# Optimization experiments

Hardware: AMD Instinct MI355X
Metric: run time of the kernel (lower is better)

## Reference

```python
import jax, jax.numpy as jnp
import numpy as np

GROUP_SIZE = 16
E2M1_MAX = 6.0
# Positive E2M1 grid and midpoints for round-to-nearest
E2M1_POS = jnp.array([0.0, 0.5, 1.0, 1.5, 2.0, 3.0, 4.0, 6.0], jnp.float32)
E2M1_MID = jnp.array([0.25, 0.75, 1.25, 1.75, 2.5, 3.5, 5.0], jnp.float32)
# Full 16-entry signed LUT (bit3 = sign, sign-magnitude)
E2M1_LUT = jnp.array([0.0, 0.5, 1.0, 1.5, 2.0, 3.0, 4.0, 6.0,
                      -0.0, -0.5, -1.0, -1.5, -2.0, -3.0, -4.0, -6.0], jnp.float32)

def _round_e2m1(x):
    # nearest value on the E2M1 grid (clamped to +-6)
    idx = jnp.searchsorted(E2M1_MID, jnp.abs(x))
    return jnp.sign(x) * E2M1_POS[idx]

def nvfp4_act_qdq(x, input_scale):
    # per-group dynamic quantize to NVFP4 with fp8-e4m3 group scale, then dequantize
    orig_shape = x.shape
    xg = x.astype(jnp.float32).reshape(*orig_shape[:-1], -1, GROUP_SIZE)
    amax = jnp.max(jnp.abs(xg), axis=-1, keepdims=True)
    s = (amax / (E2M1_MAX * input_scale)).astype(jnp.float8_e4m3fn).astype(jnp.float32)
    s = jnp.where(s > 0, s, 1.0)
    total = s * input_scale  # effective per-group scale
    dq = _round_e2m1(xg / total) * total
    return dq.reshape(orig_shape).astype(jnp.float16)

def nvfp4_dequantize(weight, weight_scale, weight_scale_2):
    # weight: [O, I//2] packed bytes (values 0..255); low nibble = even index
    O = weight.shape[0]
    low = weight & 0xF
    high = (weight >> 4) & 0xF
    codes = jnp.stack([low, high], axis=-1).reshape(O, -1)  # [O, I]
    vals = E2M1_LUT[codes].reshape(O, -1, GROUP_SIZE)       # [O, G, 16]
    w = vals * weight_scale[:, :, None] * weight_scale_2
    return w.reshape(O, -1).astype(jnp.float16)

def setup_inputs() -> dict:
    key = jax.random.key(0)
    k1, k2, k3 = jax.random.split(key, 3)
    B, S, I, O = 8, 16, 8192, 8192
    hidden_states = jax.random.normal(k1, (B, S, I), dtype=jnp.float16)
    weight = jax.random.randint(k2, (O, I // 2), 0, 256, dtype=jnp.int32)
    weight_scale = jax.random.uniform(k3, (O, I // GROUP_SIZE), dtype=jnp.float32) * 0.05 + 0.001
    weight_scale_2 = jnp.ones((1,), jnp.float32)
    input_scale = jnp.ones((1,), jnp.float32)
    return {"hidden_states": hidden_states, "weight": weight,
            "weight_scale": weight_scale, "weight_scale_2": weight_scale_2,
            "input_scale": input_scale}

def reference(hidden_states, weight, weight_scale, weight_scale_2, input_scale):
    hs_dq = nvfp4_act_qdq(hidden_states, input_scale)
    w_dq = nvfp4_dequantize(weight, weight_scale, weight_scale_2)
    return jnp.matmul(hs_dq, w_dq.T)  # [B, S, O], fp16
```

## Files before the change

kernel.cpp:

```cpp
#include <hip/hip_runtime.h>
#include <stdint.h>


typedef _Float16 half8 __attribute__((ext_vector_type(8)));
typedef float float4v __attribute__((ext_vector_type(4)));

__device__ __forceinline__ uint32_t perm_b32(uint32_t hi, uint32_t lo, uint32_t sel) {
  return __builtin_amdgcn_perm(hi, lo, sel);
}

__device__ __forceinline__ float e4m3_roundtrip(float x) {
  if (x < 0.015625f) {
    return __builtin_rintf(x * 512.0f) * 0.001953125f;
  }
  uint32_t u = __float_as_uint(x);
  u += 0x7FFFFu + ((u >> 20) & 1u);
  u &= 0xFFF00000u;
  float y = __uint_as_float(u);
  return fminf(y, 448.0f);
}

__global__ __launch_bounds__(256)
void aqdq_kernel(const float* __restrict__ hs,
                 const float* __restrict__ isc,
                 uint4* __restrict__ asw) {
  const int t = blockIdx.x * 256 + threadIdx.x;
  const int m = t >> 9;
  const int g = t & 511;
  const float* p = hs + m * 8192 + g * 16;
  float x[16];
#pragma unroll
  for (int q = 0; q < 4; ++q) *(float4*)&x[q * 4] = ((const float4*)p)[q];
  float amax = 0.0f;
#pragma unroll
  for (int i = 0; i < 16; ++i) amax = fmaxf(amax, fabsf(x[i]));

  float is = isc[0];
  float s = e4m3_roundtrip(amax / (6.0f * is));
  if (!(s > 0.0f)) s = 1.0f;
  float total = s * is;

  union { _Float16 h[16]; uint4 v4[2]; } qq;
#pragma unroll
  for (int i = 0; i < 16; ++i) {
    float r = x[i] / total;
    float a = fabsf(r);
    float v = (a <= 0.25f) ? 0.0f
            : (a <= 0.75f) ? 0.5f
            : (a <= 1.25f) ? 1.0f
            : (a <= 1.75f) ? 1.5f
            : (a <= 2.5f)  ? 2.0f
            : (a <= 3.5f)  ? 3.0f
            : (a <= 5.0f)  ? 4.0f : 6.0f;
    qq.h[i] = (_Float16)(copysignf(v, r) * total);
  }
  const int mb = m >> 4;
#pragma unroll
  for (int hf = 0; hf < 2; ++hf) {
    int k = g * 16 + hf * 8;
    int kb = k >> 5;
    int quad = (k >> 3) & 3;
    int lane = (m & 15) | (quad << 4);
    asw[(kb * 8 + mb) * 64 + lane] = qq.v4[hf];
  }
}

__device__ __forceinline__ half8 decode_scale(int4 w, float sf) {
  uint32_t t0 = perm_b32((uint32_t)w.y, (uint32_t)w.x, 0x00000400u);
  uint32_t t1 = perm_b32((uint32_t)w.w, (uint32_t)w.z, 0x04000000u);
  uint32_t b  = perm_b32(t1, t0, 0x07060100u);
  uint32_t ev = b & 0x0F0F0F0Fu;
  uint32_t od = (b >> 4) & 0x0F0F0F0Fu;
  uint32_t evm = ev & 0x07070707u;
  uint32_t odm = od & 0x07070707u;
  uint32_t evs = (ev & 0x08080808u) << 4;
  uint32_t ods = (od & 0x08080808u) << 4;
  uint32_t evh = perm_b32(0x46444240u, 0x3E3C3800u, evm) | evs;
  uint32_t odh = perm_b32(0x46444240u, 0x3E3C3800u, odm) | ods;
  union { uint32_t u[4]; half8 h; } r;
  r.u[0] = perm_b32(odh, evh, 0x04000000u) & 0xFF00FF00u;
  r.u[1] = perm_b32(odh, evh, 0x05000100u) & 0xFF00FF00u;
  r.u[2] = perm_b32(odh, evh, 0x06000200u) & 0xFF00FF00u;
  r.u[3] = perm_b32(odh, evh, 0x07000300u) & 0xFF00FF00u;
  _Float16 hsf = (_Float16)sf;
  half8 sv = {hsf, hsf, hsf, hsf, hsf, hsf, hsf, hsf};
  return r.h * sv;
}

__global__ __launch_bounds__(512)
void gemm_kernel(const uint4* __restrict__ asw,
                 const int* __restrict__ wq,
                 const float* __restrict__ wsc,
                 const float* __restrict__ ws2p,
                 float* __restrict__ out) {
  __shared__ float red[8][32][136];
  const int lane = threadIdx.x & 63;
  const int wv = threadIdx.x >> 6;
  const int quad = lane >> 4;
  const int n0 = blockIdx.x * 32;
  const int rA = n0 + (lane & 15);
  const int rB = rA + 16;
  const float ws2 = ws2p[0];
  const int4* wpA = (const int4*)(wq + rA * 4096);
  const int4* wpB = (const int4*)(wq + rB * 4096);
  const float* wsA = wsc + rA * 512;
  const float* wsB = wsc + rB * 512;
  const int kbase = wv * 1024;

  float4v acc[2][8];
#pragma unroll
  for (int ng = 0; ng < 2; ++ng)
#pragma unroll
    for (int mb = 0; mb < 8; ++mb) acc[ng][mb] = (float4v){0.f, 0.f, 0.f, 0.f};

  const uint4* ap = asw + (kbase >> 5) * 512 + lane;

#pragma unroll 2
  for (int ks = 0; ks < 32; ++ks) {
    const int k0 = kbase + ks * 32;
    const int wi = (k0 >> 3) + quad;
    int4 wA = wpA[wi];
    int4 wB = wpB[wi];
    const int si = (k0 >> 4) + (quad >> 1);
    float sA = wsA[si] * ws2;
    float sB = wsB[si] * ws2;
    uint4 af[8];
#pragma unroll
    for (int mb = 0; mb < 8; ++mb) af[mb] = ap[ks * 512 + mb * 64];
    half8 bA = decode_scale(wA, sA);
    half8 bB = decode_scale(wB, sB);
#pragma unroll
    for (int mb = 0; mb < 8; ++mb) {
      union { uint4 u; half8 h; } a;
      a.u = af[mb];
      acc[0][mb] = __builtin_amdgcn_mfma_f32_16x16x32_f16(a.h, bA, acc[0][mb], 0, 0, 0);
      acc[1][mb] = __builtin_amdgcn_mfma_f32_16x16x32_f16(a.h, bB, acc[1][mb], 0, 0, 0);
    }
  }

#pragma unroll
  for (int ng = 0; ng < 2; ++ng)
#pragma unroll
    for (int mb = 0; mb < 8; ++mb) {
      *(float4v*)&red[wv][ng * 16 + (lane & 15)][mb * 16 + quad * 4] = acc[ng][mb];
    }
  __syncthreads();

  const int t = threadIdx.x;
  const int m = t >> 2;
  const int ng8 = (t & 3) * 8;
  float o[8];
#pragma unroll
  for (int j = 0; j < 8; ++j) {
    float s = 0.f;
#pragma unroll
    for (int p = 0; p < 8; ++p) s += red[p][ng8 + j][m];
    o[j] = s;
  }
  float* op = out + m * 8192 + n0 + ng8;
  *(float4*)&op[0] = *(float4*)&o[0];
  *(float4*)&op[4] = *(float4*)&o[4];
}

extern "C" void kernel_launch(void* const* d_in, const int* in_sizes, int n_in,
                              void* d_out, int out_size, void* d_ws, size_t ws_size,
                              hipStream_t stream) {
  (void)in_sizes; (void)n_in; (void)out_size; (void)ws_size;
  const float* hs  = (const float*)d_in[0];
  const int* wq    = (const int*)d_in[1];
  const float* wsc = (const float*)d_in[2];
  const float* ws2 = (const float*)d_in[3];
  const float* isc = (const float*)d_in[4];
  float* out       = (float*)d_out;
  uint4* asw       = (uint4*)d_ws;

  aqdq_kernel<<<256, 256, 0, stream>>>(hs, isc, asw);
  gemm_kernel<<<256, 512, 0, stream>>>(asw, wq, wsc, ws2, out);
}
```

Baseline: 252.2 us.

## Software-pipeline GEMM main loop with register prefetch and nontemporal weight loads

Restructures the GEMM k-loop into a manually software-pipelined form. Weights and scales are prefetched four steps ahead and activation fragments two steps ahead in rotating register buffers, so global-load latency overlaps the MFMA work. Weight loads use nontemporal hints, and launch bounds now request two blocks per CU. The extra prefetch buffers raise register pressure, which under the occupancy hint could cause spills.

```diff
diff --git a/kernel.cpp b/kernel.cpp
--- a/kernel.cpp
+++ b/kernel.cpp
@@ -4,6 +4,8 @@
 
 typedef _Float16 half8 __attribute__((ext_vector_type(8)));
 typedef float float4v __attribute__((ext_vector_type(4)));
+typedef int int4v __attribute__((ext_vector_type(4)));
+typedef unsigned int uint4v __attribute__((ext_vector_type(4)));
 
 __device__ __forceinline__ uint32_t perm_b32(uint32_t hi, uint32_t lo, uint32_t sel) {
   return __builtin_amdgcn_perm(hi, lo, sel);
@@ -65,7 +67,7 @@
   }
 }
 
-__device__ __forceinline__ half8 decode_scale(int4 w, float sf) {
+__device__ __forceinline__ half8 decode_scale(int4v w, float sf) {
   uint32_t t0 = perm_b32((uint32_t)w.y, (uint32_t)w.x, 0x00000400u);
   uint32_t t1 = perm_b32((uint32_t)w.w, (uint32_t)w.z, 0x04000000u);
   uint32_t b  = perm_b32(t1, t0, 0x07060100u);
@@ -87,7 +89,7 @@
   return r.h * sv;
 }
 
-__global__ __launch_bounds__(512)
+__global__ __launch_bounds__(512, 2)
 void gemm_kernel(const uint4* __restrict__ asw,
                  const int* __restrict__ wq,
                  const float* __restrict__ wsc,
@@ -97,15 +99,18 @@
   const int lane = threadIdx.x & 63;
   const int wv = threadIdx.x >> 6;
   const int quad = lane >> 4;
+  const int qh = quad >> 1;
   const int n0 = blockIdx.x * 32;
   const int rA = n0 + (lane & 15);
   const int rB = rA + 16;
   const float ws2 = ws2p[0];
-  const int4* wpA = (const int4*)(wq + rA * 4096);
-  const int4* wpB = (const int4*)(wq + rB * 4096);
+  const int4v* wpA = (const int4v*)(wq + (size_t)rA * 4096);
+  const int4v* wpB = (const int4v*)(wq + (size_t)rB * 4096);
   const float* wsA = wsc + rA * 512;
   const float* wsB = wsc + rB * 512;
   const int kbase = wv * 1024;
+  const int kb8 = kbase >> 3;
+  const int kb16 = kbase >> 4;
 
   float4v acc[2][8];
 #pragma unroll
@@ -113,30 +118,55 @@
 #pragma unroll
     for (int mb = 0; mb < 8; ++mb) acc[ng][mb] = (float4v){0.f, 0.f, 0.f, 0.f};
 
-  const uint4* ap = asw + (kbase >> 5) * 512 + lane;
-
-#pragma unroll 2
-  for (int ks = 0; ks < 32; ++ks) {
-    const int k0 = kbase + ks * 32;
-    const int wi = (k0 >> 3) + quad;
-    int4 wA = wpA[wi];
-    int4 wB = wpB[wi];
-    const int si = (k0 >> 4) + (quad >> 1);
-    float sA = wsA[si] * ws2;
-    float sB = wsB[si] * ws2;
-    uint4 af[8];
-#pragma unroll
-    for (int mb = 0; mb < 8; ++mb) af[mb] = ap[ks * 512 + mb * 64];
-    half8 bA = decode_scale(wA, sA);
-    half8 bB = decode_scale(wB, sB);
-#pragma unroll
-    for (int mb = 0; mb < 8; ++mb) {
-      union { uint4 u; half8 h; } a;
-      a.u = af[mb];
-      acc[0][mb] = __builtin_amdgcn_mfma_f32_16x16x32_f16(a.h, bA, acc[0][mb], 0, 0, 0);
-      acc[1][mb] = __builtin_amdgcn_mfma_f32_16x16x32_f16(a.h, bB, acc[1][mb], 0, 0, 0);
-    }
-  }
+  const uint4v* ap = (const uint4v*)asw + (kbase >> 5) * 512 + lane;
+
+  int4v wAb[4], wBb[4];
+  float sAb[4], sBb[4];
+  uint4v afb[2][8];
+
+#define H_LOAD_W(j, ks) { \
+    int wi_ = kb8 + (ks) * 4 + quad; \
+    wAb[j] = __builtin_nontemporal_load(wpA + wi_); \
+    wBb[j] = __builtin_nontemporal_load(wpB + wi_); \
+    int si_ = kb16 + (ks) * 2 + qh; \
+    sAb[j] = wsA[si_] * ws2; \
+    sBb[j] = wsB[si_] * ws2; }
+
+#define H_LOAD_A(j, ks) { \
+    _Pragma("unroll") \
+    for (int mb_ = 0; mb_ < 8; ++mb_) afb[j][mb_] = ap[(ks) * 512 + mb_ * 64]; }
+
+#define H_COMP(aj, wj) { \
+    half8 bA_ = decode_scale(wAb[wj], sAb[wj]); \
+    half8 bB_ = decode_scale(wBb[wj], sBb[wj]); \
+    _Pragma("unroll") \
+    for (int mb_ = 0; mb_ < 8; ++mb_) { \
+      union { uint4v u; half8 h; } a_; a_.u = afb[aj][mb_]; \
+      acc[0][mb_] = __builtin_amdgcn_mfma_f32_16x16x32_f16(a_.h, bA_, acc[0][mb_], 0, 0, 0); \
+      acc[1][mb_] = __builtin_amdgcn_mfma_f32_16x16x32_f16(a_.h, bB_, acc[1][mb_], 0, 0, 0); } }
+
+  H_LOAD_A(0, 0);
+  H_LOAD_A(1, 1);
+  H_LOAD_W(0, 0);
+  H_LOAD_W(1, 1);
+  H_LOAD_W(2, 2);
+  H_LOAD_W(3, 3);
+
+#pragma unroll 1
+  for (int kc = 0; kc < 28; kc += 4) {
+    H_COMP(0, 0); H_LOAD_A(0, kc + 2); H_LOAD_W(0, kc + 4);
+    H_COMP(1, 1); H_LOAD_A(1, kc + 3); H_LOAD_W(1, kc + 5);
+    H_COMP(0, 2); H_LOAD_A(0, kc + 4); H_LOAD_W(2, kc + 6);
+    H_COMP(1, 3); H_LOAD_A(1, kc + 5); H_LOAD_W(3, kc + 7);
+  }
+  H_COMP(0, 0); H_LOAD_A(0, 30);
+  H_COMP(1, 1); H_LOAD_A(1, 31);
+  H_COMP(0, 2);
+  H_COMP(1, 3);
+
+#undef H_LOAD_W
+#undef H_LOAD_A
+#undef H_COMP
 
 #pragma unroll
   for (int ng = 0; ng < 2; ++ng)
```

Result: slower. 345.6 us (+37.0%).
